# Optimization experiments

Hardware: AMD Instinct MI355X
Metric: run time of the kernel (lower is better)

## Reference

```python
import jax, jax.numpy as jnp
import numpy as np

CUTOFF = 3.5          # angular_cutoff (init kwarg)
EPS = 1e-7            # keras.backend.epsilon()
CLIP_MIN = 1e-10      # tf.clip_by_value min on Carnot denominators
B, N = 8, 32
MLP_DIMS = [(9, 64), (64, 64), (64, 64), (64, 64), (64, 64), (64, 128), (128, 256)]


def _he(key, fan_in, fan_out):
    return jax.random.normal(key, (fan_in, fan_out), jnp.float32) * np.float32(np.sqrt(2.0 / fan_in))


def setup_inputs() -> dict:
    key = jax.random.key(0)
    k_pos, k_sp, k_w, k_b = jax.random.split(key, 4)
    # realistic symmetric distance matrix with zero diagonal, from random 3D positions
    pos = jax.random.uniform(k_pos, (B, N, 3), jnp.float32) * 9.0
    diff = pos[:, :, None, :] - pos[:, None, :, :]
    D = jnp.sqrt(jnp.sum(diff * diff, axis=-1) + 1e-12)
    D = D * (1.0 - jnp.eye(N, dtype=jnp.float32))
    species = jax.random.randint(k_sp, (B, N), 1, 10).astype(jnp.float32)
    inp = {"distance_matrices": D, "num_species_batch": species}
    for i, (fi, fo) in enumerate(MLP_DIMS):
        inp[f"W{i}"] = _he(jax.random.fold_in(k_w, i), fi, fo)
        inp[f"b{i}"] = jax.random.normal(jax.random.fold_in(k_b, i), (fo,), jnp.float32) * 0.01
    return inp


def _ang_mlp(x, W0, b0, W1, b1, W2, b2, W3, b3, W4, b4, W5, b5, W6, b6):
    # residual MLP: 9 -> 64 (x5, two residual adds) -> 128 -> 256, all tanh
    x_res = jnp.tanh(x @ W0 + b0)
    x1 = jnp.tanh(x_res @ W1 + b1)
    xb1 = x1 + x_res
    x2 = jnp.tanh(xb1 @ W2 + b2)
    x3 = jnp.tanh(x2 @ W3 + b3)
    x4 = jnp.tanh(x3 @ W4 + b4)
    xb2 = x4 + xb1
    xb3 = jnp.tanh(xb2 @ W5 + b5)
    return jnp.tanh(xb3 @ W6 + b6)


def _forward(D, S, W0, b0, W1, b1, W2, b2, W3, b3, W4, b4, W5, b5, W6, b6):
    n = D.shape[-1]
    ji, ki = jnp.triu_indices(n, k=1)                       # P = n(n-1)/2 ordered pairs j<k
    cm = (D < CUTOFF) & (D != 0.0)                          # [B,N,N]
    mask = cm[:, :, ji] & cm[:, :, ki]                      # [B,N,P] valid triplets (i;j,k)
    R_ij = D[:, :, ji]                                      # [B,N,P]
    R_ik = D[:, :, ki]
    R_jk = jnp.broadcast_to(D[:, ji, ki][:, None, :], R_ij.shape)
    z_i = jnp.broadcast_to(S[:, :, None], R_ij.shape)
    z_j = jnp.broadcast_to(S[:, ji][:, None, :], R_ij.shape)
    z_k = jnp.broadcast_to(S[:, ki][:, None, :], R_ij.shape)
    # Carnot formula for the three cosines of the triangle (i,j,k)
    clip = lambda d: jnp.maximum(d, CLIP_MIN)
    c_i = (R_ij**2 + R_ik**2 - R_jk**2) / clip(2.0 * R_ij * R_ik)
    c_j = (R_ij**2 + R_jk**2 - R_ik**2) / clip(2.0 * R_ij * R_jk)
    c_k = (R_ik**2 + R_jk**2 - R_ij**2) / clip(2.0 * R_ik * R_jk)
    geo = jnp.stack([
        R_ij + R_ik + R_jk,
        R_ij * R_ik + R_ij * R_jk + R_ik * R_jk,
        R_ij * R_ik * R_jk,
    ], axis=-1)                                             # [B,N,P,3]
    chem = jnp.stack([
        z_i + z_j + z_k,
        c_i + c_j + c_k,
        z_i * (z_j + z_k) + z_j * z_k - c_i * (c_j + c_k) - c_j * c_k,
        z_i * (c_j + c_k) + c_i * (z_j + z_k) + z_j * c_k + c_j * z_k,
        z_i * (z_j * z_k - c_j * c_k) - c_i * (z_j * c_k + c_j * z_k),
        z_i * (z_j * c_k + c_j * z_k) + c_i * (z_j * z_k - c_j * c_k),
    ], axis=-1)                                             # [B,N,P,6]
    geo = geo / (jnp.linalg.norm(geo, axis=-1, keepdims=True) + EPS)
    chem = chem / (jnp.linalg.norm(chem, axis=-1, keepdims=True) + EPS)
    feat = jnp.concatenate([geo, chem], axis=-1)            # [B,N,P,9]
    out = _ang_mlp(feat, W0, b0, W1, b1, W2, b2, W3, b3, W4, b4, W5, b5, W6, b6)  # [B,N,P,256]
    f_c = lambda d: 0.5 * jnp.cos(np.float32(np.pi) * d / CUTOFF) + 0.5
    w = jnp.where(mask, f_c(R_ij) * f_c(R_ik), 0.0)[..., None]
    GA = jnp.sum(out * w, axis=2)                           # scatter-add over triplets -> [B,N,256]
    return GA / (jnp.linalg.norm(GA, axis=-1, keepdims=True) + EPS)


def reference(distance_matrices, num_species_batch, W0, b0, W1, b1, W2, b2, W3, b3, W4, b4, W5, b5, W6, b6):
    return _forward(distance_matrices, num_species_batch, W0, b0, W1, b1, W2, b2, W3, b3, W4, b4, W5, b5, W6, b6)
```

## Files before the change

### kernel.cpp

```cpp
#include <hip/hip_runtime.h>
#include <math.h>

#define NB 8
#define NA 32
#define NCELL 256
#define NPAIR 496
#define SLOT 496
#define FST 10
#define TC 16
#define XS 20
#define NQ 8
#define CUTOFF_F 3.5f
#define EPS_F 1e-7f
#define CLIP_MIN_F 1e-10f
#define PI_F 3.14159274101257324f

#define PIPE_BAR4() do { \
    asm volatile("s_waitcnt lgkmcnt(0) vmcnt(4)" ::: "memory"); \
    __builtin_amdgcn_s_barrier(); \
    __builtin_amdgcn_sched_barrier(0); \
} while (0)
#define PIPE_BAR0() do { \
    asm volatile("s_waitcnt lgkmcnt(0) vmcnt(0)" ::: "memory"); \
    __builtin_amdgcn_s_barrier(); \
    __builtin_amdgcn_sched_barrier(0); \
} while (0)

__device__ __forceinline__ float fast_tanh(float x) {
    const float ax = fabsf(x);
    const float t = exp2f(fminf(2.8853900817779268f * ax, 30.0f));
    const float r = (t - 1.0f) * __builtin_amdgcn_rcpf(t + 1.0f);
    return __int_as_float((__float_as_int(x) & 0x80000000) | __float_as_int(r));
}

__global__ __launch_bounds__(256) void aev_feat(
    const float* __restrict__ D, const float* __restrict__ S,
    float* __restrict__ feat, int* __restrict__ count, float* __restrict__ GA)
{
    __shared__ float Dm[NA][NA];
    __shared__ float Sv[NA];
    __shared__ int s_T;
    const int tid = threadIdx.x;
    const int cell = blockIdx.x;
    const int b = cell >> 5, i = cell & 31;

    for (int idx = tid; idx < NA * NA; idx += 256)
        ((float*)Dm)[idx] = D[b * NA * NA + idx];
    if (tid < NA) Sv[tid] = S[b * NA + tid];
    if (tid == 0) s_T = 0;
    GA[cell * 256 + tid] = 0.f;
    __syncthreads();

    for (int p = tid; p < NPAIR; p += 256) {
        int rem = p, j = 0;
        while (rem >= 31 - j) { rem -= 31 - j; ++j; }
        const int k = j + 1 + rem;
        const float dij = Dm[i][j], dik = Dm[i][k];
        if (dij < CUTOFF_F && dij != 0.f && dik < CUTOFF_F && dik != 0.f) {
            const int slot = atomicAdd(&s_T, 1);
            const float Rij = dij, Rik = dik, Rjk = Dm[j][k];
            const float zi = Sv[i], zj = Sv[j], zk = Sv[k];
            const float ci = (Rij*Rij + Rik*Rik - Rjk*Rjk) / fmaxf(2.f*Rij*Rik, CLIP_MIN_F);
            const float cj = (Rij*Rij + Rjk*Rjk - Rik*Rik) / fmaxf(2.f*Rij*Rjk, CLIP_MIN_F);
            const float ck = (Rik*Rik + Rjk*Rjk - Rij*Rij) / fmaxf(2.f*Rik*Rjk, CLIP_MIN_F);
            float g0 = Rij + Rik + Rjk;
            float g1 = Rij*Rik + Rij*Rjk + Rik*Rjk;
            float g2 = Rij*Rik*Rjk;
            const float gn = sqrtf(g0*g0 + g1*g1 + g2*g2) + EPS_F;
            float h0 = zi + zj + zk;
            float h1 = ci + cj + ck;
            float h2 = zi*(zj + zk) + zj*zk - ci*(cj + ck) - cj*ck;
            float h3 = zi*(cj + ck) + ci*(zj + zk) + zj*ck + cj*zk;
            float h4 = zi*(zj*zk - cj*ck) - ci*(zj*ck + cj*zk);
            float h5 = zi*(zj*ck + cj*zk) + ci*(zj*zk - cj*ck);
            const float hn = sqrtf(h0*h0 + h1*h1 + h2*h2 + h3*h3 + h4*h4 + h5*h5) + EPS_F;
            const float fcij = 0.5f * cosf(PI_F * Rij / CUTOFF_F) + 0.5f;
            const float fcik = 0.5f * cosf(PI_F * Rik / CUTOFF_F) + 0.5f;
            float* fp = &feat[(cell * SLOT + slot) * FST];
            fp[0] = g0 / gn; fp[1] = g1 / gn; fp[2] = g2 / gn;
            fp[3] = h0 / hn; fp[4] = h1 / hn; fp[5] = h2 / hn;
            fp[6] = h3 / hn; fp[7] = h4 / hn; fp[8] = h5 / hn;
            fp[9] = fcij * fcik;
        }
    }
    __syncthreads();
    if (tid == 0) count[cell] = s_T;
}

__device__ __forceinline__ void cp_async16(const float* g, float* l) {
    __builtin_amdgcn_global_load_lds(
        (const __attribute__((address_space(1))) unsigned int*)g,
        (__attribute__((address_space(3))) unsigned int*)l, 16, 0, 0);
}

__device__ __forceinline__ void stage16k(const float* __restrict__ g,
                                         float* __restrict__ buf, int tid) {
    const int lane = tid & 63, w = tid >> 6;
#pragma unroll
    for (int r = 0; r < 4; ++r) {
        const int off = (w * 4 + r) * 256;
        cp_async16(g + off + lane * 4, buf + off);
    }
}

template<int K, bool RES>
__device__ __forceinline__ void compute64(
    const float* __restrict__ Wl, float bb,
    const float* __restrict__ X, float* __restrict__ Y,
    const float* __restrict__ R, int tid)
{
    const int fi = tid & 63;
    const int xo = (tid >> 6) * 4;
    float a0 = bb, a1 = bb, a2 = bb, a3 = bb;
#pragma unroll 4
    for (int k = 0; k < K; ++k) {
        const float4 xv = *(const float4*)&X[k * XS + xo];
        const float w = Wl[k * 64 + fi];
        a0 += xv.x * w; a1 += xv.y * w; a2 += xv.z * w; a3 += xv.w * w;
    }
    float4 y;
    y.x = fast_tanh(a0); y.y = fast_tanh(a1); y.z = fast_tanh(a2); y.w = fast_tanh(a3);
    if (RES) {
        const float4 r = *(const float4*)&R[fi * XS + xo];
        y.x += r.x; y.y += r.y; y.z += r.z; y.w += r.w;
    }
    *(float4*)&Y[fi * XS + xo] = y;
}

__device__ __forceinline__ void compute5_part(
    const float* __restrict__ Wl , const float* __restrict__ X,
    int k0, float (&a0)[4], float (&a1)[4], int tid)
{
    const int fo = tid & 63;
    const int xo = (tid >> 6) * 4;
#pragma unroll 4
    for (int k = 0; k < 32; ++k) {
        const float4 xv = *(const float4*)&X[(k0 + k) * XS + xo];
        const float w0 = Wl[k * 128 + fo];
        const float w1 = Wl[k * 128 + fo + 64];
        a0[0] += xv.x * w0; a0[1] += xv.y * w0; a0[2] += xv.z * w0; a0[3] += xv.w * w0;
        a1[0] += xv.x * w1; a1[1] += xv.y * w1; a1[2] += xv.z * w1; a1[3] += xv.w * w1;
    }
}

__device__ __forceinline__ void compute6_part(
    const float* __restrict__ Wl , const float* __restrict__ X,
    float (&a)[16], int tid)
{
#pragma unroll 2
    for (int k = 0; k < 16; ++k) {
        const float w = Wl[k * 256 + tid];
        const float4 x0 = *(const float4*)&X[k * XS + 0];
        const float4 x1 = *(const float4*)&X[k * XS + 4];
        const float4 x2 = *(const float4*)&X[k * XS + 8];
        const float4 x3 = *(const float4*)&X[k * XS + 12];
        a[0]  += x0.x * w; a[1]  += x0.y * w; a[2]  += x0.z * w; a[3]  += x0.w * w;
        a[4]  += x1.x * w; a[5]  += x1.y * w; a[6]  += x1.z * w; a[7]  += x1.w * w;
        a[8]  += x2.x * w; a[9]  += x2.y * w; a[10] += x2.z * w; a[11] += x2.w * w;
        a[12] += x3.x * w; a[13] += x3.y * w; a[14] += x3.z * w; a[15] += x3.w * w;
    }
}

__global__ __launch_bounds__(256) void aev_mlp(
    const float* __restrict__ feat, const int* __restrict__ count,
    const float* __restrict__ W0, const float* __restrict__ b0,
    const float* __restrict__ W1, const float* __restrict__ b1,
    const float* __restrict__ W2, const float* __restrict__ b2,
    const float* __restrict__ W3, const float* __restrict__ b3,
    const float* __restrict__ W4, const float* __restrict__ b4,
    const float* __restrict__ W5, const float* __restrict__ b5,
    const float* __restrict__ W6, const float* __restrict__ b6,
    float* __restrict__ GA)
{
    __shared__ __align__(16) float WB0[4096];
    __shared__ __align__(16) float WB1[4096];
    __shared__ __align__(16) float WB2[4096];
    __shared__ __align__(16) float W0s[576];
    __shared__ __align__(16) float Xs[9 * XS];
    __shared__ __align__(16) float U0[64 * XS];
    __shared__ __align__(16) float U1[64 * XS];
    __shared__ __align__(16) float U2[64 * XS];
    __shared__ float wsh[TC];

    const int tid = threadIdx.x;
    const int cell = blockIdx.x & 255;
    const int q = blockIdx.x >> 8;
    const int T = count[cell];
    const int nch = (T + TC - 1) / TC;
    if (q >= nch) return;

    const int fi64 = tid & 63;
    const float bias0 = b0[fi64];
    const float bias1 = b1[fi64];
    const float bias2 = b2[fi64];
    const float bias3 = b3[fi64];
    const float bias4 = b4[fi64];
    const float bias5a = b5[fi64];
    const float bias5b = b5[fi64 + 64];
    const float bias6 = b6[tid];

    if (tid < 144) ((float4*)W0s)[tid] = ((const float4*)W0)[tid];

    float gacc = 0.f;

    for (int c = q; c < nch; c += NQ) {
        const int t0 = c * TC;

        stage16k(W1, WB0, tid);
        if (tid < TC * FST) {
            const int t = tid / FST, qf = tid % FST;
            const int slot = t0 + t;
            const float v = (slot < T) ? feat[(cell * SLOT + t0) * FST + tid] : 0.f;
            if (qf == 9) wsh[t] = v; else Xs[qf * XS + t] = v;
        }
        PIPE_BAR4();
        stage16k(W2, WB1, tid);
        compute64<9,  false>(W0s, bias0, Xs, U0, nullptr, tid);
        PIPE_BAR4();
        stage16k(W3, WB2, tid);
        compute64<64, true >(WB0, bias1, U0, U1, U0, tid);
        PIPE_BAR4();
        stage16k(W4, WB0, tid);
        compute64<64, false>(WB1, bias2, U1, U2, nullptr, tid);
        PIPE_BAR4();
        stage16k(W5, WB1, tid);
        compute64<64, false>(WB2, bias3, U2, U0, nullptr, tid);
        PIPE_BAR4();
        stage16k(W5 + 4096, WB2, tid);
        compute64<64, true >(WB0, bias4, U0, U2, U1, tid);
        PIPE_BAR4();

        float a0[4], a1[4];
#pragma unroll
        for (int r = 0; r < 4; ++r) { a0[r] = bias5a; a1[r] = bias5b; }
        stage16k(W6, WB0, tid);
        compute5_part(WB1, U2, 0, a0, a1, tid);
        PIPE_BAR4();
        stage16k(W6 + 4096, WB1, tid);
        compute5_part(WB2, U2, 32, a0, a1, tid);
        {
            const int fo = tid & 63;
            const int xo = (tid >> 6) * 4;
            float4 y0, y1;
            y0.x = fast_tanh(a0[0]); y0.y = fast_tanh(a0[1]);
            y0.z = fast_tanh(a0[2]); y0.w = fast_tanh(a0[3]);
            y1.x = fast_tanh(a1[0]); y1.y = fast_tanh(a1[1]);
            y1.z = fast_tanh(a1[2]); y1.w = fast_tanh(a1[3]);
            *(float4*)&U0[fo * XS + xo] = y0;
            *(float4*)&U1[fo * XS + xo] = y1;
        }
        PIPE_BAR4();

        float a6[16];
#pragma unroll
        for (int r = 0; r < 16; ++r) a6[r] = bias6;
        stage16k(W6 + 2 * 4096, WB2, tid);
        compute6_part(WB0, U0 + 0 * XS, a6, tid);
        PIPE_BAR4();
        stage16k(W6 + 3 * 4096, WB0, tid);
        compute6_part(WB1, U0 + 16 * XS, a6, tid);
        PIPE_BAR4();
        stage16k(W6 + 4 * 4096, WB1, tid);
        compute6_part(WB2, U0 + 32 * XS, a6, tid);
        PIPE_BAR4();
        stage16k(W6 + 5 * 4096, WB2, tid);
        compute6_part(WB0, U0 + 48 * XS, a6, tid);
        PIPE_BAR4();
        stage16k(W6 + 6 * 4096, WB0, tid);
        compute6_part(WB1, U1 + 0 * XS, a6, tid);
        PIPE_BAR4();
        stage16k(W6 + 7 * 4096, WB1, tid);
        compute6_part(WB2, U1 + 16 * XS, a6, tid);
        PIPE_BAR4();
        compute6_part(WB0, U1 + 32 * XS, a6, tid);
        PIPE_BAR0();
        compute6_part(WB1, U1 + 48 * XS, a6, tid);

#pragma unroll 4
        for (int r = 0; r < 16; ++r)
            gacc += wsh[r] * fast_tanh(a6[r]);
        __syncthreads();
    }

    atomicAdd(&GA[cell * 256 + tid], gacc);
}

__global__ __launch_bounds__(256) void aev_norm(
    const float* __restrict__ GA, float* __restrict__ out)
{
    __shared__ float wred[4];
    const int tid = threadIdx.x;
    const int cell = blockIdx.x;
    const float v = GA[cell * 256 + tid];
    float ss = v * v;
#pragma unroll
    for (int off = 32; off > 0; off >>= 1) ss += __shfl_down(ss, off);
    if ((tid & 63) == 0) wred[tid >> 6] = ss;
    __syncthreads();
    const float tot = wred[0] + wred[1] + wred[2] + wred[3];
    out[cell * 256 + tid] = v / (sqrtf(tot) + EPS_F);
}

extern "C" void kernel_launch(void* const* d_in, const int* in_sizes, int n_in,
                              void* d_out, int out_size, void* d_ws, size_t ws_size,
                              hipStream_t stream)
{
    const float* D  = (const float*)d_in[0];
    const float* S  = (const float*)d_in[1];
    const float* W0 = (const float*)d_in[2];  const float* b0 = (const float*)d_in[3];
    const float* W1 = (const float*)d_in[4];  const float* b1 = (const float*)d_in[5];
    const float* W2 = (const float*)d_in[6];  const float* b2 = (const float*)d_in[7];
    const float* W3 = (const float*)d_in[8];  const float* b3 = (const float*)d_in[9];
    const float* W4 = (const float*)d_in[10]; const float* b4 = (const float*)d_in[11];
    const float* W5 = (const float*)d_in[12]; const float* b5 = (const float*)d_in[13];
    const float* W6 = (const float*)d_in[14]; const float* b6 = (const float*)d_in[15];
    float* out = (float*)d_out;

    float* feat  = (float*)d_ws;
    int*   count = (int*)(feat + NCELL * SLOT * FST);
    float* GA    = (float*)(count + 256);

    aev_feat<<<dim3(NCELL), dim3(256), 0, stream>>>(D, S, feat, count, GA);
    aev_mlp<<<dim3(NCELL * NQ), dim3(256), 0, stream>>>(
        feat, count, W0, b0, W1, b1, W2, b2, W3, b3, W4, b4, W5, b5, W6, b6, GA);
    aev_norm<<<dim3(NCELL), dim3(256), 0, stream>>>(GA, out);
}
```

Baseline: 115.9 us.

## Fuse triplet feature computation into MLP kernel and drop global atomics

Removes the separate feature kernel. Each MLP block now loads the distance matrix, builds a ballot bitmask of valid triplets, and computes its chunk's 16 features on the fly by finding the r-th set bit, so the global feature buffer and count array are no longer needed. Per-block partial sums go to separate slots that the norm kernel adds up, replacing global atomicAdd and the zero-init. This saves a launch and a global round-trip, but every one of the NQ blocks per cell repeats the D load and mask build, and feature work is serialized on 16 threads.

```diff
diff --git a/kernel.cpp b/kernel.cpp
--- a/kernel.cpp
+++ b/kernel.cpp
@@ -5,8 +5,6 @@
 #define NA 32
 #define NCELL 256
 #define NPAIR 496
-#define SLOT 496
-#define FST 10
 #define TC 16
 #define XS 20
 #define NQ 8
@@ -33,60 +31,6 @@
     return __int_as_float((__float_as_int(x) & 0x80000000) | __float_as_int(r));
 }
 
-__global__ __launch_bounds__(256) void aev_feat(
-    const float* __restrict__ D, const float* __restrict__ S,
-    float* __restrict__ feat, int* __restrict__ count, float* __restrict__ GA)
-{
-    __shared__ float Dm[NA][NA];
-    __shared__ float Sv[NA];
-    __shared__ int s_T;
-    const int tid = threadIdx.x;
-    const int cell = blockIdx.x;
-    const int b = cell >> 5, i = cell & 31;
-
-    for (int idx = tid; idx < NA * NA; idx += 256)
-        ((float*)Dm)[idx] = D[b * NA * NA + idx];
-    if (tid < NA) Sv[tid] = S[b * NA + tid];
-    if (tid == 0) s_T = 0;
-    GA[cell * 256 + tid] = 0.f;
-    __syncthreads();
-
-    for (int p = tid; p < NPAIR; p += 256) {
-        int rem = p, j = 0;
-        while (rem >= 31 - j) { rem -= 31 - j; ++j; }
-        const int k = j + 1 + rem;
-        const float dij = Dm[i][j], dik = Dm[i][k];
-        if (dij < CUTOFF_F && dij != 0.f && dik < CUTOFF_F && dik != 0.f) {
-            const int slot = atomicAdd(&s_T, 1);
-            const float Rij = dij, Rik = dik, Rjk = Dm[j][k];
-            const float zi = Sv[i], zj = Sv[j], zk = Sv[k];
-            const float ci = (Rij*Rij + Rik*Rik - Rjk*Rjk) / fmaxf(2.f*Rij*Rik, CLIP_MIN_F);
-            const float cj = (Rij*Rij + Rjk*Rjk - Rik*Rik) / fmaxf(2.f*Rij*Rjk, CLIP_MIN_F);
-            const float ck = (Rik*Rik + Rjk*Rjk - Rij*Rij) / fmaxf(2.f*Rik*Rjk, CLIP_MIN_F);
-            float g0 = Rij + Rik + Rjk;
-            float g1 = Rij*Rik + Rij*Rjk + Rik*Rjk;
-            float g2 = Rij*Rik*Rjk;
-            const float gn = sqrtf(g0*g0 + g1*g1 + g2*g2) + EPS_F;
-            float h0 = zi + zj + zk;
-            float h1 = ci + cj + ck;
-            float h2 = zi*(zj + zk) + zj*zk - ci*(cj + ck) - cj*ck;
-            float h3 = zi*(cj + ck) + ci*(zj + zk) + zj*ck + cj*zk;
-            float h4 = zi*(zj*zk - cj*ck) - ci*(zj*ck + cj*zk);
-            float h5 = zi*(zj*ck + cj*zk) + ci*(zj*zk - cj*ck);
-            const float hn = sqrtf(h0*h0 + h1*h1 + h2*h2 + h3*h3 + h4*h4 + h5*h5) + EPS_F;
-            const float fcij = 0.5f * cosf(PI_F * Rij / CUTOFF_F) + 0.5f;
-            const float fcik = 0.5f * cosf(PI_F * Rik / CUTOFF_F) + 0.5f;
-            float* fp = &feat[(cell * SLOT + slot) * FST];
-            fp[0] = g0 / gn; fp[1] = g1 / gn; fp[2] = g2 / gn;
-            fp[3] = h0 / hn; fp[4] = h1 / hn; fp[5] = h2 / hn;
-            fp[6] = h3 / hn; fp[7] = h4 / hn; fp[8] = h5 / hn;
-            fp[9] = fcij * fcik;
-        }
-    }
-    __syncthreads();
-    if (tid == 0) count[cell] = s_T;
-}
-
 __device__ __forceinline__ void cp_async16(const float* g, float* l) {
     __builtin_amdgcn_global_load_lds(
         (const __attribute__((address_space(1))) unsigned int*)g,
@@ -101,6 +45,12 @@
         const int off = (w * 4 + r) * 256;
         cp_async16(g + off + lane * 4, buf + off);
     }
+}
+
+__device__ __forceinline__ void decode_pair(int p, int& j, int& k) {
+    int rem = p; j = 0;
+    while (rem >= 31 - j) { rem -= 31 - j; ++j; }
+    k = j + 1 + rem;
 }
 
 template<int K, bool RES>
@@ -162,7 +112,7 @@
 }
 
 __global__ __launch_bounds__(256) void aev_mlp(
-    const float* __restrict__ feat, const int* __restrict__ count,
+    const float* __restrict__ D, const float* __restrict__ S,
     const float* __restrict__ W0, const float* __restrict__ b0,
     const float* __restrict__ W1, const float* __restrict__ b1,
     const float* __restrict__ W2, const float* __restrict__ b2,
@@ -170,12 +120,15 @@
     const float* __restrict__ W4, const float* __restrict__ b4,
     const float* __restrict__ W5, const float* __restrict__ b5,
     const float* __restrict__ W6, const float* __restrict__ b6,
-    float* __restrict__ GA)
+    float* __restrict__ GAq)
 {
     __shared__ __align__(16) float WB0[4096];
     __shared__ __align__(16) float WB1[4096];
     __shared__ __align__(16) float WB2[4096];
     __shared__ __align__(16) float W0s[576];
+    __shared__ __align__(16) float Dm[NA][NA];
+    __shared__ float Sv[NA];
+    __shared__ unsigned long long msk[8];
     __shared__ __align__(16) float Xs[9 * XS];
     __shared__ __align__(16) float U0[64 * XS];
     __shared__ __align__(16) float U1[64 * XS];
@@ -185,9 +138,41 @@
     const int tid = threadIdx.x;
     const int cell = blockIdx.x & 255;
     const int q = blockIdx.x >> 8;
-    const int T = count[cell];
+    const int b = cell >> 5, i = cell & 31;
+    float* gslot = &GAq[(cell * NQ + q) * 256];
+
+    for (int idx = tid; idx < NA * NA; idx += 256)
+        ((float*)Dm)[idx] = D[b * NA * NA + idx];
+    if (tid < NA) Sv[tid] = S[b * NA + tid];
+    __syncthreads();
+
+    {
+        int j, k;
+        decode_pair(tid, j, k);
+        const float dij = Dm[i][j], dik = Dm[i][k];
+        const bool f0 = (dij < CUTOFF_F) & (dij != 0.f) & (dik < CUTOFF_F) & (dik != 0.f);
+        const unsigned long long m0 = __ballot(f0);
+        if ((tid & 63) == 0) msk[tid >> 6] = m0;
+        bool f1 = false;
+        const int p1 = tid + 256;
+        if (p1 < NPAIR) {
+            decode_pair(p1, j, k);
+            const float a = Dm[i][j], c = Dm[i][k];
+            f1 = (a < CUTOFF_F) & (a != 0.f) & (c < CUTOFF_F) & (c != 0.f);
+        }
+        const unsigned long long m1 = __ballot(f1);
+        if ((tid & 63) == 0) msk[4 + (tid >> 6)] = m1;
+    }
+    __syncthreads();
+
+    int T = 0;
+#pragma unroll
+    for (int w = 0; w < 8; ++w) T += __popcll(msk[w]);
     const int nch = (T + TC - 1) / TC;
-    if (q >= nch) return;
+    if (q >= nch) {
+        gslot[tid] = 0.f;
+        return;
+    }
 
     const int fi64 = tid & 63;
     const float bias0 = b0[fi64];
@@ -204,14 +189,51 @@
     float gacc = 0.f;
 
     for (int c = q; c < nch; c += NQ) {
-        const int t0 = c * TC;
-
         stage16k(W1, WB0, tid);
-        if (tid < TC * FST) {
-            const int t = tid / FST, qf = tid % FST;
-            const int slot = t0 + t;
-            const float v = (slot < T) ? feat[(cell * SLOT + t0) * FST + tid] : 0.f;
-            if (qf == 9) wsh[t] = v; else Xs[qf * XS + t] = v;
+        if (tid < TC) {
+            float f9[9];
+#pragma unroll
+            for (int u = 0; u < 9; ++u) f9[u] = 0.f;
+            float wcut = 0.f;
+            const int r = c * TC + tid;
+            if (r < T) {
+                int rr = r, word = 0;
+                while (true) {
+                    const int pc = __popcll(msk[word]);
+                    if (rr < pc) break;
+                    rr -= pc; ++word;
+                }
+                unsigned long long m = msk[word];
+                for (int s = 0; s < rr; ++s) m &= m - 1;
+                const int p = word * 64 + (__ffsll((long long)m) - 1);
+                int j, k;
+                decode_pair(p, j, k);
+                const float Rij = Dm[i][j], Rik = Dm[i][k], Rjk = Dm[j][k];
+                const float zi = Sv[i], zj = Sv[j], zk = Sv[k];
+                const float ci = (Rij*Rij + Rik*Rik - Rjk*Rjk) / fmaxf(2.f*Rij*Rik, CLIP_MIN_F);
+                const float cj = (Rij*Rij + Rjk*Rjk - Rik*Rik) / fmaxf(2.f*Rij*Rjk, CLIP_MIN_F);
+                const float ck = (Rik*Rik + Rjk*Rjk - Rij*Rij) / fmaxf(2.f*Rik*Rjk, CLIP_MIN_F);
+                float g0 = Rij + Rik + Rjk;
+                float g1 = Rij*Rik + Rij*Rjk + Rik*Rjk;
+                float g2 = Rij*Rik*Rjk;
+                const float gn = sqrtf(g0*g0 + g1*g1 + g2*g2) + EPS_F;
+                float h0 = zi + zj + zk;
+                float h1 = ci + cj + ck;
+                float h2 = zi*(zj + zk) + zj*zk - ci*(cj + ck) - cj*ck;
+                float h3 = zi*(cj + ck) + ci*(zj + zk) + zj*ck + cj*zk;
+                float h4 = zi*(zj*zk - cj*ck) - ci*(zj*ck + cj*zk);
+                float h5 = zi*(zj*ck + cj*zk) + ci*(zj*zk - cj*ck);
+                const float hn = sqrtf(h0*h0 + h1*h1 + h2*h2 + h3*h3 + h4*h4 + h5*h5) + EPS_F;
+                f9[0] = g0 / gn; f9[1] = g1 / gn; f9[2] = g2 / gn;
+                f9[3] = h0 / hn; f9[4] = h1 / hn; f9[5] = h2 / hn;
+                f9[6] = h3 / hn; f9[7] = h4 / hn; f9[8] = h5 / hn;
+                const float fcij = 0.5f * cosf(PI_F * Rij / CUTOFF_F) + 0.5f;
+                const float fcik = 0.5f * cosf(PI_F * Rik / CUTOFF_F) + 0.5f;
+                wcut = fcij * fcik;
+            }
+#pragma unroll
+            for (int u = 0; u < 9; ++u) Xs[u * XS + tid] = f9[u];
+            wsh[tid] = wcut;
         }
         PIPE_BAR4();
         stage16k(W2, WB1, tid);
@@ -282,16 +304,19 @@
         __syncthreads();
     }
 
-    atomicAdd(&GA[cell * 256 + tid], gacc);
+    gslot[tid] = gacc;
 }
 
 __global__ __launch_bounds__(256) void aev_norm(
-    const float* __restrict__ GA, float* __restrict__ out)
+    const float* __restrict__ GAq, float* __restrict__ out)
 {
     __shared__ float wred[4];
     const int tid = threadIdx.x;
     const int cell = blockIdx.x;
-    const float v = GA[cell * 256 + tid];
+    float v = 0.f;
+#pragma unroll
+    for (int q = 0; q < NQ; ++q)
+        v += GAq[(cell * NQ + q) * 256 + tid];
     float ss = v * v;
 #pragma unroll
     for (int off = 32; off > 0; off >>= 1) ss += __shfl_down(ss, off);
@@ -316,12 +341,9 @@
     const float* W6 = (const float*)d_in[14]; const float* b6 = (const float*)d_in[15];
     float* out = (float*)d_out;
 
-    float* feat  = (float*)d_ws;
-    int*   count = (int*)(feat + NCELL * SLOT * FST);
-    float* GA    = (float*)(count + 256);
-
-    aev_feat<<<dim3(NCELL), dim3(256), 0, stream>>>(D, S, feat, count, GA);
+    float* GAq = (float*)d_ws;
+
     aev_mlp<<<dim3(NCELL * NQ), dim3(256), 0, stream>>>(
-        feat, count, W0, b0, W1, b1, W2, b2, W3, b3, W4, b4, W5, b5, W6, b6, GA);
-    aev_norm<<<dim3(NCELL), dim3(256), 0, stream>>>(GA, out);
-}
+        D, S, W0, b0, W1, b1, W2, b2, W3, b3, W4, b4, W5, b5, W6, b6, GAq);
+    aev_norm<<<dim3(NCELL), dim3(256), 0, stream>>>(GAq, out);
+}
```

Result: slower. 134.8 us (+16.4%).

## Register-tile the last two MLP layers as 4x2 and 4x4 outer products

Applied to the files above, without the earlier changes.

Layers 5 and 6 now give each thread a small 2D register tile of features by triplets, built from float4 weight loads and float2/float4 activation loads. Before, each thread owned one or two features and broadcast-read all activations. This cuts LDS reads per FMA in the dominant 128->256 layer. Because layer-6 outputs for one feature are now spread over four threads, the weighted triplet sum goes through a shared-memory buffer (U2) with an extra barrier before accumulating into gacc.

```diff
diff --git a/kernel.cpp b/kernel.cpp
--- a/kernel.cpp
+++ b/kernel.cpp
@@ -129,35 +129,33 @@
 
 __device__ __forceinline__ void compute5_part(
     const float* __restrict__ Wl , const float* __restrict__ X,
-    int k0, float (&a0)[4], float (&a1)[4], int tid)
-{
-    const int fo = tid & 63;
-    const int xo = (tid >> 6) * 4;
+    int k0, float (&a)[4][2], int tid)
+{
+    const int f = (tid & 31) * 4;
+    const int t = (tid >> 5) * 2;
 #pragma unroll 4
     for (int k = 0; k < 32; ++k) {
-        const float4 xv = *(const float4*)&X[(k0 + k) * XS + xo];
-        const float w0 = Wl[k * 128 + fo];
-        const float w1 = Wl[k * 128 + fo + 64];
-        a0[0] += xv.x * w0; a0[1] += xv.y * w0; a0[2] += xv.z * w0; a0[3] += xv.w * w0;
-        a1[0] += xv.x * w1; a1[1] += xv.y * w1; a1[2] += xv.z * w1; a1[3] += xv.w * w1;
+        const float4 wv = *(const float4*)&Wl[k * 128 + f];
+        const float2 xv = *(const float2*)&X[(k0 + k) * XS + t];
+        a[0][0] += wv.x * xv.x; a[0][1] += wv.x * xv.y;
+        a[1][0] += wv.y * xv.x; a[1][1] += wv.y * xv.y;
+        a[2][0] += wv.z * xv.x; a[2][1] += wv.z * xv.y;
+        a[3][0] += wv.w * xv.x; a[3][1] += wv.w * xv.y;
     }
 }
 
 __device__ __forceinline__ void compute6_part(
     const float* __restrict__ Wl , const float* __restrict__ X,
-    float (&a)[16], int tid)
+    float (&c)[4][4], int f, int t)
 {
 #pragma unroll 2
     for (int k = 0; k < 16; ++k) {
-        const float w = Wl[k * 256 + tid];
-        const float4 x0 = *(const float4*)&X[k * XS + 0];
-        const float4 x1 = *(const float4*)&X[k * XS + 4];
-        const float4 x2 = *(const float4*)&X[k * XS + 8];
-        const float4 x3 = *(const float4*)&X[k * XS + 12];
-        a[0]  += x0.x * w; a[1]  += x0.y * w; a[2]  += x0.z * w; a[3]  += x0.w * w;
-        a[4]  += x1.x * w; a[5]  += x1.y * w; a[6]  += x1.z * w; a[7]  += x1.w * w;
-        a[8]  += x2.x * w; a[9]  += x2.y * w; a[10] += x2.z * w; a[11] += x2.w * w;
-        a[12] += x3.x * w; a[13] += x3.y * w; a[14] += x3.z * w; a[15] += x3.w * w;
+        const float4 wv = *(const float4*)&Wl[k * 256 + f];
+        const float4 xv = *(const float4*)&X[k * XS + t];
+        c[0][0] += wv.x * xv.x; c[0][1] += wv.x * xv.y; c[0][2] += wv.x * xv.z; c[0][3] += wv.x * xv.w;
+        c[1][0] += wv.y * xv.x; c[1][1] += wv.y * xv.y; c[1][2] += wv.y * xv.z; c[1][3] += wv.y * xv.w;
+        c[2][0] += wv.z * xv.x; c[2][1] += wv.z * xv.y; c[2][2] += wv.z * xv.z; c[2][3] += wv.z * xv.w;
+        c[3][0] += wv.w * xv.x; c[3][1] += wv.w * xv.y; c[3][2] += wv.w * xv.z; c[3][3] += wv.w * xv.w;
     }
 }
 
@@ -195,9 +193,12 @@
     const float bias2 = b2[fi64];
     const float bias3 = b3[fi64];
     const float bias4 = b4[fi64];
-    const float bias5a = b5[fi64];
-    const float bias5b = b5[fi64 + 64];
-    const float bias6 = b6[tid];
+    const int f5 = (tid & 31) * 4;
+    const int t5 = (tid >> 5) * 2;
+    const float4 bias5v = *(const float4*)&b5[f5];
+    const int f6 = (tid >> 6) * 64 + (tid & 15) * 4;
+    const int t6 = ((tid >> 4) & 3) * 4;
+    const float4 bias6v = *(const float4*)&b6[f6];
 
     if (tid < 144) ((float4*)W0s)[tid] = ((const float4*)W0)[tid];
 
@@ -230,55 +231,78 @@
         compute64<64, true >(WB0, bias4, U0, U2, U1, tid);
         PIPE_BAR4();
 
-        float a0[4], a1[4];
-#pragma unroll
-        for (int r = 0; r < 4; ++r) { a0[r] = bias5a; a1[r] = bias5b; }
+        float a5[4][2];
+#pragma unroll
+        for (int i = 0; i < 4; ++i) {
+            const float bi = (i == 0) ? bias5v.x : (i == 1) ? bias5v.y
+                           : (i == 2) ? bias5v.z : bias5v.w;
+            a5[i][0] = bi; a5[i][1] = bi;
+        }
         stage16k(W6, WB0, tid);
-        compute5_part(WB1, U2, 0, a0, a1, tid);
+        compute5_part(WB1, U2, 0, a5, tid);
         PIPE_BAR4();
         stage16k(W6 + 4096, WB1, tid);
-        compute5_part(WB2, U2, 32, a0, a1, tid);
+        compute5_part(WB2, U2, 32, a5, tid);
         {
-            const int fo = tid & 63;
-            const int xo = (tid >> 6) * 4;
-            float4 y0, y1;
-            y0.x = fast_tanh(a0[0]); y0.y = fast_tanh(a0[1]);
-            y0.z = fast_tanh(a0[2]); y0.w = fast_tanh(a0[3]);
-            y1.x = fast_tanh(a1[0]); y1.y = fast_tanh(a1[1]);
-            y1.z = fast_tanh(a1[2]); y1.w = fast_tanh(a1[3]);
-            *(float4*)&U0[fo * XS + xo] = y0;
-            *(float4*)&U1[fo * XS + xo] = y1;
-        }
-        PIPE_BAR4();
-
-        float a6[16];
-#pragma unroll
-        for (int r = 0; r < 16; ++r) a6[r] = bias6;
+            float* base = (f5 < 64) ? U0 : U1;
+            const int fr = f5 & 63;
+#pragma unroll
+            for (int i = 0; i < 4; ++i) {
+                float2 y;
+                y.x = fast_tanh(a5[i][0]); y.y = fast_tanh(a5[i][1]);
+                *(float2*)&base[(fr + i) * XS + t5] = y;
+            }
+        }
+        PIPE_BAR4();
+
+        float c6[4][4];
+#pragma unroll
+        for (int i = 0; i < 4; ++i) {
+            const float bi = (i == 0) ? bias6v.x : (i == 1) ? bias6v.y
+                           : (i == 2) ? bias6v.z : bias6v.w;
+#pragma unroll
+            for (int j = 0; j < 4; ++j) c6[i][j] = bi;
+        }
         stage16k(W6 + 2 * 4096, WB2, tid);
-        compute6_part(WB0, U0 + 0 * XS, a6, tid);
+        compute6_part(WB0, U0 + 0 * XS, c6, f6, t6);
         PIPE_BAR4();
         stage16k(W6 + 3 * 4096, WB0, tid);
-        compute6_part(WB1, U0 + 16 * XS, a6, tid);
+        compute6_part(WB1, U0 + 16 * XS, c6, f6, t6);
         PIPE_BAR4();
         stage16k(W6 + 4 * 4096, WB1, tid);
-        compute6_part(WB2, U0 + 32 * XS, a6, tid);
+        compute6_part(WB2, U0 + 32 * XS, c6, f6, t6);
         PIPE_BAR4();
         stage16k(W6 + 5 * 4096, WB2, tid);
-        compute6_part(WB0, U0 + 48 * XS, a6, tid);
+        compute6_part(WB0, U0 + 48 * XS, c6, f6, t6);
         PIPE_BAR4();
         stage16k(W6 + 6 * 4096, WB0, tid);
-        compute6_part(WB1, U1 + 0 * XS, a6, tid);
+        compute6_part(WB1, U1 + 0 * XS, c6, f6, t6);
         PIPE_BAR4();
         stage16k(W6 + 7 * 4096, WB1, tid);
-        compute6_part(WB2, U1 + 16 * XS, a6, tid);
-        PIPE_BAR4();
-        compute6_part(WB0, U1 + 32 * XS, a6, tid);
+        compute6_part(WB2, U1 + 16 * XS, c6, f6, t6);
+        PIPE_BAR4();
+        compute6_part(WB0, U1 + 32 * XS, c6, f6, t6);
         PIPE_BAR0();
-        compute6_part(WB1, U1 + 48 * XS, a6, tid);
-
-#pragma unroll 4
-        for (int r = 0; r < 16; ++r)
-            gacc += wsh[r] * fast_tanh(a6[r]);
+        compute6_part(WB1, U1 + 48 * XS, c6, f6, t6);
+
+        {
+            const float4 wv4 = *(const float4*)&wsh[t6];
+            float4 s;
+            s.x = wv4.x * fast_tanh(c6[0][0]) + wv4.y * fast_tanh(c6[0][1])
+                + wv4.z * fast_tanh(c6[0][2]) + wv4.w * fast_tanh(c6[0][3]);
+            s.y = wv4.x * fast_tanh(c6[1][0]) + wv4.y * fast_tanh(c6[1][1])
+                + wv4.z * fast_tanh(c6[1][2]) + wv4.w * fast_tanh(c6[1][3]);
+            s.z = wv4.x * fast_tanh(c6[2][0]) + wv4.y * fast_tanh(c6[2][1])
+                + wv4.z * fast_tanh(c6[2][2]) + wv4.w * fast_tanh(c6[2][3]);
+            s.w = wv4.x * fast_tanh(c6[3][0]) + wv4.y * fast_tanh(c6[3][1])
+                + wv4.z * fast_tanh(c6[3][2]) + wv4.w * fast_tanh(c6[3][3]);
+            *(float4*)&U2[((f6 >> 2) << 4) + (t6 & 12)] = s;
+        }
+        __syncthreads();
+        gacc += U2[(tid >> 2) * 16 + 0  + (tid & 3)]
+              + U2[(tid >> 2) * 16 + 4  + (tid & 3)]
+              + U2[(tid >> 2) * 16 + 8  + (tid & 3)]
+              + U2[(tid >> 2) * 16 + 12 + (tid & 3)];
         __syncthreads();
     }
 
```

Result: no change. 115.3 us (median of 2 runs) (-0.5%).
